# Kernel tuning notes

Measured on AMD Instinct MI355X. Metric: run time of the kernel, lower is better.

The kernel has to match this reference:

```python
import jax, jax.numpy as jnp
import numpy as np

D_IN = 1024
D_OUT = 1024
NUM_HEADS = 16
DIM_HEAD = D_OUT // NUM_HEADS


def setup_inputs() -> dict:
    key = jax.random.key(0)
    ks = jax.random.split(key, 6)
    s = 0.02
    x = jax.random.normal(ks[0], (2, 2048, D_IN), dtype=jnp.float32)
    Wk = jax.random.normal(ks[1], (D_IN, D_OUT), dtype=jnp.float32) * s
    Wq = jax.random.normal(ks[2], (D_IN, D_OUT), dtype=jnp.float32) * s
    Wv = jax.random.normal(ks[3], (D_IN, D_OUT), dtype=jnp.float32) * s
    Wo = jax.random.normal(ks[4], (D_OUT, D_OUT), dtype=jnp.float32) * s
    bo = jax.random.normal(ks[5], (D_OUT,), dtype=jnp.float32) * s
    return {"x": x, "Wk": Wk, "Wq": Wq, "Wv": Wv, "Wo": Wo, "bo": bo}


def reference(x, Wk, Wq, Wv, Wo, bo):
    B, S, _ = x.shape
    # projections -> [B, H, S, Dh]
    def split_heads(t):
        return t.reshape(B, S, NUM_HEADS, DIM_HEAD).transpose(0, 2, 1, 3)
    q = split_heads(x @ Wq)
    k = split_heads(x @ Wk)
    v = split_heads(x @ Wv)
    # NOTE: source uses non-in-place masked_fill whose result is discarded,
    # so NO causal mask is actually applied (faithful reproduction).
    scores = jnp.einsum("bhqd,bhkd->bhqk", q, k) / jnp.sqrt(jnp.float32(DIM_HEAD))
    wgts = jax.nn.softmax(scores, axis=-1)  # dropout = identity (eval mode)
    ctx = jnp.einsum("bhqk,bhkd->bhqd", wgts, v)
    ctx = ctx.transpose(0, 2, 1, 3).reshape(B, S, D_OUT)
    return ctx @ Wo + bo
```

## Files before the change

kernel.cpp:

```cpp
#include <hip/hip_runtime.h>
#include <stdint.h>

typedef short bf16x8 __attribute__((ext_vector_type(8)));
typedef short s16x4  __attribute__((ext_vector_type(4)));
typedef float f32x4  __attribute__((ext_vector_type(4)));
typedef unsigned int u32x4 __attribute__((ext_vector_type(4)));
typedef unsigned int u32x2 __attribute__((ext_vector_type(2)));

__device__ __forceinline__ unsigned short f2bf(float f) {
  unsigned int u = __builtin_bit_cast(unsigned int, f) + 0x8000u;
  return (unsigned short)(u >> 16);
}
__device__ __forceinline__ unsigned int pack2bf(float a, float b) {
  unsigned int ua = __builtin_bit_cast(unsigned int, a) + 0x8000u;
  unsigned int ub = __builtin_bit_cast(unsigned int, b) + 0x8000u;
  return __builtin_amdgcn_perm(ub, ua, 0x07060302);
}

__device__ __forceinline__ void gl2lds16(const void* g, void* l) {
  __builtin_amdgcn_global_load_lds(
      (const __attribute__((address_space(1))) void*)g,
      (__attribute__((address_space(3))) void*)l, 16, 0, 0);
}

__global__ __launch_bounds__(256) void cast_x_k(const float* __restrict__ x,
                                                unsigned short* __restrict__ xb) {
  int i = blockIdx.x * 256 + threadIdx.x;
  float4 v = ((const float4*)x)[i];
  u32x2 o;
  o.x = pack2bf(v.x, v.y);
  o.y = pack2bf(v.z, v.w);
  ((u32x2*)xb)[i] = o;
}

__global__ __launch_bounds__(256) void castT_k(
    const float* __restrict__ Wq, const float* __restrict__ Wk,
    const float* __restrict__ Wv, const float* __restrict__ Wo,
    unsigned short* __restrict__ Tq, unsigned short* __restrict__ Tk,
    unsigned short* __restrict__ Tv, unsigned short* __restrict__ To) {
  __shared__ float tile[32][33];
  const int z = blockIdx.z;
  const float* W = (z == 0) ? Wq : (z == 1) ? Wk : (z == 2) ? Wv : Wo;
  unsigned short* T = (z == 0) ? Tq : (z == 1) ? Tk : (z == 2) ? Tv : To;
  const int tx = threadIdx.x, ty = threadIdx.y;
  const int n0 = blockIdx.x * 32, k0 = blockIdx.y * 32;
#pragma unroll
  for (int j = 0; j < 32; j += 8)
    tile[ty + j][tx] = W[(size_t)(k0 + ty + j) * 1024 + n0 + tx];
  __syncthreads();
#pragma unroll
  for (int j = 0; j < 32; j += 8)
    T[(size_t)(n0 + ty + j) * 1024 + k0 + tx] = f2bf(tile[tx][ty + j]);
}

template <int MODE, int TN>
__global__ __launch_bounds__(256) void gemm_bt_k(const unsigned short* __restrict__ A,
                                                 const unsigned short* __restrict__ B,
                                                 void* __restrict__ C,
                                                 const float* __restrict__ bias,
                                                 int K) {
  __shared__ alignas(16) short lA[1024 * 8];
  __shared__ alignas(16) short lB[256 * TN * 8];
  const int tid = threadIdx.x;
  const int wid = tid >> 6, lane = tid & 63;
  const int l15 = lane & 15, quad = lane >> 4;
  const int waveM = wid >> 1, waveN = wid & 1;
  const int bm = blockIdx.y * 128, bn = blockIdx.x * (32 * TN);

  f32x4 acc[4][TN];
#pragma unroll
  for (int i = 0; i < 4; ++i)
#pragma unroll
    for (int j = 0; j < TN; ++j) acc[i][j] = (f32x4){0.f, 0.f, 0.f, 0.f};

  for (int kk = 0; kk < K; kk += 64) {
    __syncthreads();
#pragma unroll
    for (int j = 0; j < 4; ++j) {
      int c = tid + 256 * j;
      int row = ((c >> 7) << 4) | (c & 15);
      int ch = (c >> 4) & 7;
      gl2lds16(A + (size_t)(bm + row) * K + kk + ch * 8, &lA[(c & ~63) * 8]);
    }
#pragma unroll
    for (int j = 0; j < TN; ++j) {
      int c = tid + 256 * j;
      int row = ((c >> 7) << 4) | (c & 15);
      int ch = (c >> 4) & 7;
      gl2lds16(B + (size_t)(bn + row) * K + kk + ch * 8, &lB[(c & ~63) * 8]);
    }
    __syncthreads();
#pragma unroll
    for (int ks = 0; ks < 2; ++ks) {
      bf16x8 af[4], bfr[TN];
#pragma unroll
      for (int i = 0; i < 4; ++i)
        af[i] = *(bf16x8*)&lA[(((waveM * 4 + i) * 2 + ks) * 64 + lane) * 8];
#pragma unroll
      for (int j = 0; j < TN; ++j)
        bfr[j] = *(bf16x8*)&lB[(((waveN * TN + j) * 2 + ks) * 64 + lane) * 8];
#pragma unroll
      for (int i = 0; i < 4; ++i)
#pragma unroll
        for (int j = 0; j < TN; ++j)
          acc[i][j] = __builtin_amdgcn_mfma_f32_16x16x32_bf16(af[i], bfr[j], acc[i][j], 0, 0, 0);
    }
  }

#pragma unroll
  for (int i = 0; i < 4; ++i)
#pragma unroll
    for (int j = 0; j < TN; ++j) {
      int row = bm + waveM * 64 + i * 16 + quad * 4;
      int col = bn + (waveN * TN + j) * 16 + l15;
      if (MODE == 0) {
        unsigned short* Cq = (unsigned short*)C;
        int w = col >> 10, n1 = col & 1023;
        int h = n1 >> 6, d = n1 & 63;
        int b = row >> 11, s = row & 2047;
        int bhh = (b << 4) + h;
        if (w == 2) {
          int g = (i << 2) + quad;
          int ks2 = g >> 3, rem = g & 7;
          int pos = ((ks2 << 2) + (rem & 3)) * 8 + (rem >> 2) * 4;
          u32x2 pk;
          pk.x = pack2bf(acc[i][j][0], acc[i][j][1]);
          pk.y = pack2bf(acc[i][j][2], acc[i][j][3]);
          *(u32x2*)&Cq[(size_t)2 * 4194304 + ((size_t)bhh * 64 + d) * 2048 +
                       (s & ~63) + pos] = pk;
        } else {
          float sc = (w == 0) ? 0.18033688011112042f : 1.0f;
#pragma unroll
          for (int r = 0; r < 4; ++r)
            Cq[(size_t)w * 4194304 + ((size_t)bhh * 2048 + s + r) * 64 + d] =
                f2bf(acc[i][j][r] * sc);
        }
      } else {
#pragma unroll
        for (int r = 0; r < 4; ++r)
          ((float*)C)[(size_t)(row + r) * 1024 + col] = acc[i][j][r] + bias[col];
      }
    }
}

__global__ __launch_bounds__(128) void flash_k(const unsigned short* __restrict__ Qh,
                                               const unsigned short* __restrict__ Kh,
                                               const unsigned short* __restrict__ Vt,
                                               unsigned short* __restrict__ ctxb) {
  constexpr int SL = 2048;
  __shared__ alignas(16) short kt[2][512 * 8];
  __shared__ alignas(16) short vt[2][512 * 8];

  const int tid = threadIdx.x;
  const int wid = tid >> 6, lane = tid & 63;
  const int l15 = lane & 15, quad = lane >> 4;
  const int bh = blockIdx.y;
  const int q0 = blockIdx.x * 64 + wid * 32;

  const unsigned short* Qb = Qh + (size_t)bh * SL * 64;
  const unsigned short* Kb = Kh + (size_t)bh * SL * 64;
  const unsigned short* Vb = Vt + (size_t)bh * 64 * SL;

  bf16x8 qf[2][2];
#pragma unroll
  for (int s = 0; s < 2; ++s)
#pragma unroll
    for (int ks = 0; ks < 2; ++ks)
      qf[s][ks] = *(const bf16x8*)(Qb + (size_t)(q0 + s * 16 + l15) * 64 + ks * 32 + quad * 8);

  f32x4 o[2][4];
  f32x4 rs4[2] = {(f32x4){0.f, 0.f, 0.f, 0.f}, (f32x4){0.f, 0.f, 0.f, 0.f}};
  const f32x4 z4 = (f32x4){0.f, 0.f, 0.f, 0.f};
#pragma unroll
  for (int s = 0; s < 2; ++s)
#pragma unroll
    for (int t = 0; t < 4; ++t) o[s][t] = z4;

  auto stage = [&](int kb, short* ktb, short* vtb) {
#pragma unroll
    for (int j2 = 0; j2 < 4; ++j2) {
      int cc = tid + 128 * j2;
      int row = cc >> 3;
      int ko = (cc & 7) ^ (row & 7);
      gl2lds16(Kb + (size_t)(kb + row) * 64 + ko * 8, &ktb[(cc & ~63) * 8]);
      gl2lds16(Vb + (size_t)row * SL + kb + ko * 8, &vtb[(cc & ~63) * 8]);
    }
  };

  auto compute = [&](const short* ktb, const short* vtb) {
    f32x4 sv[2][4];
#pragma unroll
    for (int t = 0; t < 4; ++t) {
      int key = t * 16 + l15;
      bf16x8 kf0 = *(bf16x8*)&ktb[(key * 8 + (quad ^ (key & 7))) * 8];
      bf16x8 kf1 = *(bf16x8*)&ktb[(key * 8 + ((4 + quad) ^ (key & 7))) * 8];
#pragma unroll
      for (int s = 0; s < 2; ++s) {
        sv[s][t] = __builtin_amdgcn_mfma_f32_16x16x32_bf16(kf0, qf[s][0], z4, 0, 0, 0);
        sv[s][t] = __builtin_amdgcn_mfma_f32_16x16x32_bf16(kf1, qf[s][1], sv[s][t], 0, 0, 0);
      }
    }
    u32x4 pf[2][2];
#pragma unroll
    for (int s = 0; s < 2; ++s)
#pragma unroll
      for (int t = 0; t < 4; ++t) {
        f32x4 p;
#pragma unroll
        for (int r = 0; r < 4; ++r) p[r] = __builtin_amdgcn_exp2f(sv[s][t][r]);
        rs4[s] += p;
        pf[s][t >> 1][(t & 1) * 2 + 0] = pack2bf(p[0], p[1]);
        pf[s][t >> 1][(t & 1) * 2 + 1] = pack2bf(p[2], p[3]);
      }
#pragma unroll
    for (int t = 0; t < 4; ++t) {
      int d = t * 16 + l15;
#pragma unroll
      for (int ks = 0; ks < 2; ++ks) {
        bf16x8 vf = *(bf16x8*)&vtb[(d * 8 + ((ks * 4 + quad) ^ (d & 7))) * 8];
#pragma unroll
        for (int s = 0; s < 2; ++s)
          o[s][t] = __builtin_amdgcn_mfma_f32_16x16x32_bf16(
              vf, __builtin_bit_cast(bf16x8, pf[s][ks]), o[s][t], 0, 0, 0);
      }
    }
  };

  stage(0, kt[0], vt[0]);
#pragma unroll 1
  for (int i2 = 0; i2 < 16; ++i2) {
    __syncthreads();
    stage((2 * i2 + 1) * 64, kt[1], vt[1]);
    compute(kt[0], vt[0]);
    __syncthreads();
    if (i2 < 15) stage((2 * i2 + 2) * 64, kt[0], vt[0]);
    compute(kt[1], vt[1]);
  }

  const int bb = bh >> 4, h = bh & 15;
#pragma unroll
  for (int s = 0; s < 2; ++s) {
    float v = (rs4[s][0] + rs4[s][1]) + (rs4[s][2] + rs4[s][3]);
    v += __shfl_xor(v, 16);
    v += __shfl_xor(v, 32);
    float inv = 1.0f / v;
    int tok = q0 + s * 16 + l15;
    size_t base = ((size_t)(bb * 2048 + tok)) * 1024 + h * 64;
#pragma unroll
    for (int t = 0; t < 4; ++t) {
      u32x2 pk;
      pk.x = pack2bf(o[s][t][0] * inv, o[s][t][1] * inv);
      pk.y = pack2bf(o[s][t][2] * inv, o[s][t][3] * inv);
      *(u32x2*)&ctxb[base + t * 16 + quad * 4] = pk;
    }
  }
}

extern "C" void kernel_launch(void* const* d_in, const int* in_sizes, int n_in,
                              void* d_out, int out_size, void* d_ws, size_t ws_size,
                              hipStream_t stream) {
  const float* x  = (const float*)d_in[0];
  const float* Wk = (const float*)d_in[1];
  const float* Wq = (const float*)d_in[2];
  const float* Wv = (const float*)d_in[3];
  const float* Wo = (const float*)d_in[4];
  const float* bo = (const float*)d_in[5];
  float* out = (float*)d_out;

  char* ws = (char*)d_ws;
  const size_t MB = 1u << 20;
  unsigned short* xb   = (unsigned short*)(ws);
  unsigned short* WqT  = (unsigned short*)(ws + 8  * MB);
  unsigned short* WkT  = (unsigned short*)(ws + 10 * MB);
  unsigned short* WvT  = (unsigned short*)(ws + 12 * MB);
  unsigned short* WoT  = (unsigned short*)(ws + 14 * MB);
  unsigned short* Qh   = (unsigned short*)(ws + 16 * MB);
  unsigned short* ctxb = xb;

  cast_x_k<<<4096, 256, 0, stream>>>(x, xb);
  castT_k<<<dim3(32, 32, 4), dim3(32, 8), 0, stream>>>(Wq, Wk, Wv, Wo, WqT, WkT, WvT, WoT);
  gemm_bt_k<0, 4><<<dim3(24, 32), 256, 0, stream>>>(xb, WqT, Qh, nullptr, 1024);
  flash_k<<<dim3(32, 32), 128, 0, stream>>>(Qh, Qh + 4194304, Qh + 2 * 4194304, ctxb);
  gemm_bt_k<1, 2><<<dim3(16, 32), 256, 0, stream>>>(ctxb, WoT, out, bo, 1024);
}
```

Baseline: 227.8 us.

## Double-buffer GEMM LDS stages and swap MFMA operands for vectorized epilogue stores

The GEMM main loop now splits each 64-wide K step into two 32-wide halves in separate LDS buffers, so global-to-LDS loads for the next half overlap MFMA work on the current one. For the Q/K projection and the output projection, the MFMA operands are swapped so each lane holds four consecutive output columns. That lets the epilogue write packed bf16 pairs or float4 rows instead of scattered scalar stores, and load the bias as a float4. V keeps the old operand order and transposed store path. The cost is more synchronisation points per K step and more code paths in the epilogue.

```diff
diff --git a/kernel.cpp b/kernel.cpp
--- a/kernel.cpp
+++ b/kernel.cpp
@@ -59,13 +59,14 @@
                                                  void* __restrict__ C,
                                                  const float* __restrict__ bias,
                                                  int K) {
-  __shared__ alignas(16) short lA[1024 * 8];
-  __shared__ alignas(16) short lB[256 * TN * 8];
+  __shared__ alignas(16) short lA[2][512 * 8];
+  __shared__ alignas(16) short lB[2][128 * TN * 8];
   const int tid = threadIdx.x;
   const int wid = tid >> 6, lane = tid & 63;
   const int l15 = lane & 15, quad = lane >> 4;
   const int waveM = wid >> 1, waveN = wid & 1;
   const int bm = blockIdx.y * 128, bn = blockIdx.x * (32 * TN);
+  const bool sw = (MODE == 1) || (bn < 2048);
 
   f32x4 acc[4][TN];
 #pragma unroll
@@ -73,53 +74,85 @@
 #pragma unroll
     for (int j = 0; j < TN; ++j) acc[i][j] = (f32x4){0.f, 0.f, 0.f, 0.f};
 
-  for (int kk = 0; kk < K; kk += 64) {
-    __syncthreads();
-#pragma unroll
-    for (int j = 0; j < 4; ++j) {
+  auto stage = [&](int kk, int bsel) {
+#pragma unroll
+    for (int j = 0; j < 2; ++j) {
       int c = tid + 256 * j;
-      int row = ((c >> 7) << 4) | (c & 15);
-      int ch = (c >> 4) & 7;
-      gl2lds16(A + (size_t)(bm + row) * K + kk + ch * 8, &lA[(c & ~63) * 8]);
-    }
-#pragma unroll
-    for (int j = 0; j < TN; ++j) {
+      int row = ((c >> 6) << 4) | (c & 15);
+      int ch = (c >> 4) & 3;
+      gl2lds16(A + (size_t)(bm + row) * K + kk + ch * 8, &lA[bsel][(c & ~63) * 8]);
+    }
+#pragma unroll
+    for (int j = 0; j < TN / 2; ++j) {
       int c = tid + 256 * j;
-      int row = ((c >> 7) << 4) | (c & 15);
-      int ch = (c >> 4) & 7;
-      gl2lds16(B + (size_t)(bn + row) * K + kk + ch * 8, &lB[(c & ~63) * 8]);
-    }
-    __syncthreads();
-#pragma unroll
-    for (int ks = 0; ks < 2; ++ks) {
-      bf16x8 af[4], bfr[TN];
+      int row = ((c >> 6) << 4) | (c & 15);
+      int ch = (c >> 4) & 3;
+      gl2lds16(B + (size_t)(bn + row) * K + kk + ch * 8, &lB[bsel][(c & ~63) * 8]);
+    }
+  };
+
+  auto compute = [&](int bsel) {
+    bf16x8 af[4], bfr[TN];
+#pragma unroll
+    for (int i = 0; i < 4; ++i)
+      af[i] = *(bf16x8*)&lA[bsel][((waveM * 4 + i) * 64 + lane) * 8];
+#pragma unroll
+    for (int j = 0; j < TN; ++j)
+      bfr[j] = *(bf16x8*)&lB[bsel][((waveN * TN + j) * 64 + lane) * 8];
+    if (sw) {
 #pragma unroll
       for (int i = 0; i < 4; ++i)
-        af[i] = *(bf16x8*)&lA[(((waveM * 4 + i) * 2 + ks) * 64 + lane) * 8];
-#pragma unroll
-      for (int j = 0; j < TN; ++j)
-        bfr[j] = *(bf16x8*)&lB[(((waveN * TN + j) * 2 + ks) * 64 + lane) * 8];
+#pragma unroll
+        for (int j = 0; j < TN; ++j)
+          acc[i][j] = __builtin_amdgcn_mfma_f32_16x16x32_bf16(bfr[j], af[i], acc[i][j], 0, 0, 0);
+    } else {
 #pragma unroll
       for (int i = 0; i < 4; ++i)
 #pragma unroll
         for (int j = 0; j < TN; ++j)
           acc[i][j] = __builtin_amdgcn_mfma_f32_16x16x32_bf16(af[i], bfr[j], acc[i][j], 0, 0, 0);
     }
+  };
+
+  stage(0, 0);
+#pragma unroll 1
+  for (int i2 = 0; i2 < K / 64; ++i2) {
+    __syncthreads();
+    stage(i2 * 64 + 32, 1);
+    compute(0);
+    __syncthreads();
+    if (i2 + 1 < K / 64) stage(i2 * 64 + 64, 0);
+    compute(1);
   }
 
-#pragma unroll
-  for (int i = 0; i < 4; ++i)
-#pragma unroll
-    for (int j = 0; j < TN; ++j) {
-      int row = bm + waveM * 64 + i * 16 + quad * 4;
-      int col = bn + (waveN * TN + j) * 16 + l15;
-      if (MODE == 0) {
-        unsigned short* Cq = (unsigned short*)C;
-        int w = col >> 10, n1 = col & 1023;
-        int h = n1 >> 6, d = n1 & 63;
-        int b = row >> 11, s = row & 2047;
-        int bhh = (b << 4) + h;
-        if (w == 2) {
+  if (MODE == 0) {
+    unsigned short* Cq = (unsigned short*)C;
+    if (sw) {
+      const int w = bn >> 10;
+      const float sc = (w == 0) ? 0.18033688011112042f : 1.0f;
+#pragma unroll
+      for (int i = 0; i < 4; ++i)
+#pragma unroll
+        for (int j = 0; j < TN; ++j) {
+          int tok = bm + waveM * 64 + i * 16 + l15;
+          int ncol = bn + (waveN * TN + j) * 16 + quad * 4;
+          int h = (ncol & 1023) >> 6, d0 = ncol & 63;
+          int bhh = ((tok >> 11) << 4) + h, s = tok & 2047;
+          u32x2 pk;
+          pk.x = pack2bf(acc[i][j][0] * sc, acc[i][j][1] * sc);
+          pk.y = pack2bf(acc[i][j][2] * sc, acc[i][j][3] * sc);
+          *(u32x2*)&Cq[(size_t)w * 4194304 + ((size_t)bhh * 2048 + s) * 64 + d0] = pk;
+        }
+    } else {
+#pragma unroll
+      for (int i = 0; i < 4; ++i)
+#pragma unroll
+        for (int j = 0; j < TN; ++j) {
+          int row = bm + waveM * 64 + i * 16 + quad * 4;
+          int col = bn + (waveN * TN + j) * 16 + l15;
+          int d = col & 63, h = (col & 1023) >> 6;
+          int b = row >> 11, s = row & 2047;
+          int bhh = (b << 4) + h;
           int g = (i << 2) + quad;
           int ks2 = g >> 3, rem = g & 7;
           int pos = ((ks2 << 2) + (rem & 3)) * 8 + (rem >> 2) * 4;
@@ -128,19 +161,24 @@
           pk.y = pack2bf(acc[i][j][2], acc[i][j][3]);
           *(u32x2*)&Cq[(size_t)2 * 4194304 + ((size_t)bhh * 64 + d) * 2048 +
                        (s & ~63) + pos] = pk;
-        } else {
-          float sc = (w == 0) ? 0.18033688011112042f : 1.0f;
-#pragma unroll
-          for (int r = 0; r < 4; ++r)
-            Cq[(size_t)w * 4194304 + ((size_t)bhh * 2048 + s + r) * 64 + d] =
-                f2bf(acc[i][j][r] * sc);
         }
-      } else {
-#pragma unroll
-        for (int r = 0; r < 4; ++r)
-          ((float*)C)[(size_t)(row + r) * 1024 + col] = acc[i][j][r] + bias[col];
+    }
+  } else {
+#pragma unroll
+    for (int i = 0; i < 4; ++i)
+#pragma unroll
+      for (int j = 0; j < TN; ++j) {
+        int tok = bm + waveM * 64 + i * 16 + l15;
+        int n0 = bn + (waveN * TN + j) * 16 + quad * 4;
+        float4 bv = *(const float4*)&bias[n0];
+        float4 ov;
+        ov.x = acc[i][j][0] + bv.x;
+        ov.y = acc[i][j][1] + bv.y;
+        ov.z = acc[i][j][2] + bv.z;
+        ov.w = acc[i][j][3] + bv.w;
+        *(float4*)&((float*)C)[(size_t)tok * 1024 + n0] = ov;
       }
-    }
+  }
 }
 
 __global__ __launch_bounds__(128) void flash_k(const unsigned short* __restrict__ Qh,
```

Measured after the change: 240.1 us. 1.05x slower.
